# Performance work log

Measured on AMD Instinct MI355X. Metric: run time of the kernel, lower is better.

## Reference

```python
import jax, jax.numpy as jnp
import numpy as np

AABB0 = np.array([-1.5, -1.5, -1.5], np.float32)
AABB1 = np.array([1.5, 1.5, 1.5], np.float32)
GRID = (300, 300, 300)
NEAR, FAR = 2.0, 6.0
STEP = float(np.mean((AABB1 - AABB0) / (np.array(GRID, np.float32) - 1)) * 0.5)  # step_ratio=0.5
DIST_SCALE = 25.0
DENSITY_SHIFT = -10.0
W_THRES = 1e-4
PE = 2  # view_pe = feat_pe = 2
MAT = ((0, 1), (0, 2), (1, 2))
VEC = (2, 1, 0)
N_RAYS, N_SAMP = 1024, 512
DN, AN = 16, 16
APP_DIM, FEAT_C = 27, 128
IN_MLP = 2 * PE * 3 + 2 * PE * APP_DIM + 3 + APP_DIM  # 150


def posenc(x, freqs):
    fb = (2.0 ** jnp.arange(freqs)).astype(x.dtype)
    p = (x[..., None] * fb).reshape(x.shape[:-1] + (x.shape[-1] * freqs,))
    return jnp.concatenate([jnp.sin(p), jnp.cos(p)], -1)


def bilinear2d(plane, xy):
    # plane [C,H,W]; xy [P,2] in [-1,1], x->W, y->H; align_corners=True, border clamp
    C, H, W = plane.shape
    x = jnp.clip((xy[:, 0] * 0.5 + 0.5) * (W - 1), 0.0, W - 1)
    y = jnp.clip((xy[:, 1] * 0.5 + 0.5) * (H - 1), 0.0, H - 1)
    x0 = jnp.clip(jnp.floor(x), 0, W - 2).astype(jnp.int32)
    y0 = jnp.clip(jnp.floor(y), 0, H - 2).astype(jnp.int32)
    wx, wy = x - x0, y - y0
    v00 = plane[:, y0, x0]
    v01 = plane[:, y0, x0 + 1]
    v10 = plane[:, y0 + 1, x0]
    v11 = plane[:, y0 + 1, x0 + 1]
    return (v00 * (1 - wx) + v01 * wx) * (1 - wy) + (v10 * (1 - wx) + v11 * wx) * wy  # [C,P]


def linear1d(line, z):
    # line [C,L]; z [P] in [-1,1]
    C, L = line.shape
    t = jnp.clip((z * 0.5 + 0.5) * (L - 1), 0.0, L - 1)
    i0 = jnp.clip(jnp.floor(t), 0, L - 2).astype(jnp.int32)
    w = t - i0
    return line[:, i0] * (1 - w) + line[:, i0 + 1] * w  # [C,P]


def _forward(rays_o, rays_d, dplanes, dlines, aplanes, alines, basis_w,
             w1, b1, w2, b2, w3, b3, n_samples):
    a0, a1 = jnp.asarray(AABB0), jnp.asarray(AABB1)
    # --- sample_ray (is_train=False) ---
    vec = jnp.where(rays_d == 0, 1e-6, rays_d)
    rate_a = (a1 - rays_o) / vec
    rate_b = (a0 - rays_o) / vec
    t_min = jnp.clip(jnp.max(jnp.minimum(rate_a, rate_b), -1), NEAR, FAR)  # [R]
    rng = jnp.arange(n_samples, dtype=rays_o.dtype)[None]
    z_vals = t_min[:, None] + STEP * rng  # [R,S]
    pts = rays_o[:, None, :] + rays_d[:, None, :] * z_vals[..., None]  # [R,S,3]
    ray_valid = jnp.all((pts >= a0) & (pts <= a1), -1)  # [R,S]
    xn = ((pts - a0) * (2.0 / (a1 - a0)) - 1.0).reshape(-1, 3)  # normalize_coord -> [P,3]
    # --- density: VM decomposition (sum of plane*line products) ---
    sigma_feat = jnp.zeros((xn.shape[0],), xn.dtype)
    for i in range(3):
        p = bilinear2d(dplanes[i], xn[:, jnp.array(MAT[i])])
        l = linear1d(dlines[i], xn[:, VEC[i]])
        sigma_feat = sigma_feat + jnp.sum(p * l, 0)
    sigma = jax.nn.softplus(sigma_feat + DENSITY_SHIFT).reshape(z_vals.shape)
    sigma = jnp.where(ray_valid, sigma, 0.0)
    # --- raw2alpha compositing ---
    dists = jnp.concatenate([z_vals[:, 1:] - z_vals[:, :-1], jnp.zeros_like(z_vals[:, :1])], -1)
    alpha = 1.0 - jnp.exp(-sigma * dists * DIST_SCALE)
    T = jnp.cumprod(jnp.concatenate([jnp.ones_like(alpha[:, :1]), 1.0 - alpha + 1e-10], -1), -1)
    weight = alpha * T[:, :-1]
    app_mask = weight > W_THRES
    # --- appearance features + basis_mat ---
    coefs = [bilinear2d(aplanes[i], xn[:, jnp.array(MAT[i])]) * linear1d(alines[i], xn[:, VEC[i]])
             for i in range(3)]
    feat = jnp.concatenate(coefs, 0).T @ basis_w.T  # [P, app_dim]
    view = jnp.broadcast_to(rays_d[:, None, :], pts.shape).reshape(-1, 3)
    # --- MLPRender_Fea: [features, viewdirs, posenc(features), posenc(viewdirs)] ---
    mlp_in = jnp.concatenate([feat, view, posenc(feat, PE), posenc(view, PE)], -1)
    h = jax.nn.relu(mlp_in @ w1.T + b1)
    h = jax.nn.relu(h @ w2.T + b2)
    rgb = jax.nn.sigmoid(h @ w3.T + b3).reshape(z_vals.shape + (3,))
    rgb = jnp.where(app_mask[..., None], rgb, 0.0)
    acc = jnp.sum(weight, -1)
    rgb_map = jnp.sum(weight[..., None] * rgb, 1)
    rgb_map = jnp.clip(rgb_map + (1.0 - acc)[:, None], 0.0, 1.0)  # white background
    depth_map = jnp.sum(weight * z_vals, -1)
    return rgb_map, depth_map


def setup_inputs() -> dict:
    key = jax.random.key(0)
    ks = jax.random.split(key, 20)
    rd = jax.random.normal(ks[0], (N_RAYS, 3), jnp.float32)
    rays_d = rd / jnp.linalg.norm(rd, axis=-1, keepdims=True)
    rays_o = -3.0 * rays_d + 0.1 * jax.random.normal(ks[1], (N_RAYS, 3), jnp.float32)
    inp = {"rays_o": rays_o, "rays_d": rays_d}
    for i, ((m0, m1), v) in enumerate(zip(MAT, VEC)):
        inp[f"dplane{i}"] = jax.random.normal(ks[2 + i], (DN, GRID[m1], GRID[m0]), jnp.float32)
        inp[f"dline{i}"] = jax.random.normal(ks[5 + i], (DN, GRID[v]), jnp.float32)
        inp[f"aplane{i}"] = 0.1 * jax.random.normal(ks[8 + i], (AN, GRID[m1], GRID[m0]), jnp.float32)
        inp[f"aline{i}"] = 0.1 * jax.random.normal(ks[11 + i], (AN, GRID[v]), jnp.float32)
    inp["basis_w"] = 0.1 * jax.random.normal(ks[14], (APP_DIM, 3 * AN), jnp.float32)
    inp["w1"] = 0.05 * jax.random.normal(ks[15], (FEAT_C, IN_MLP), jnp.float32)
    inp["b1"] = jnp.zeros((FEAT_C,), jnp.float32)
    inp["w2"] = 0.05 * jax.random.normal(ks[16], (FEAT_C, FEAT_C), jnp.float32)
    inp["b2"] = jnp.zeros((FEAT_C,), jnp.float32)
    inp["w3"] = 0.05 * jax.random.normal(ks[17], (3, FEAT_C), jnp.float32)
    inp["b3"] = jnp.zeros((3,), jnp.float32)
    inp["n_samples"] = N_SAMP
    return inp


def reference(rays_o, rays_d, dplane0, dplane1, dplane2, dline0, dline1, dline2,
              aplane0, aplane1, aplane2, aline0, aline1, aline2, basis_w,
              w1, b1, w2, b2, w3, b3, n_samples):
    return _forward(rays_o, rays_d, (dplane0, dplane1, dplane2), (dline0, dline1, dline2),
                    (aplane0, aplane1, aplane2), (aline0, aline1, aline2), basis_w,
                    w1, b1, w2, b2, w3, b3, n_samples)
```

## Files before the change

kernel.cpp:

```cpp
#include <hip/hip_runtime.h>
#include <hip/hip_fp16.h>
#include <math.h>

#define NRAYS 1024
#define NSAMP 512
#define GRIDN 300
#define POS_ELEMS (GRIDN*GRIDN)
#define PLANE_ELEMS (16*POS_ELEMS)
#define CMAX 524288

typedef short bf16x8 __attribute__((ext_vector_type(8)));
typedef short short8 __attribute__((ext_vector_type(8)));
typedef float f32x4  __attribute__((ext_vector_type(4)));

struct H8v { __half2 h[4]; };

__device__ __forceinline__ float clampf(float x, float a, float b){ return fminf(fmaxf(x,a),b); }
__device__ __forceinline__ unsigned short f2b(float f){
    unsigned u = __builtin_bit_cast(unsigned, f);
    u = (u + 0x7FFFu + ((u>>16)&1u)) >> 16;
    return (unsigned short)u;
}
__device__ __forceinline__ float b2f(unsigned short h){
    unsigned u = ((unsigned)h) << 16;
    return __builtin_bit_cast(float, u);
}

__device__ __forceinline__ float ray_tmin(float o0,float o1,float o2,float d0,float d1,float d2){
    float v0=(d0==0.f)?1e-6f:d0, v1=(d1==0.f)?1e-6f:d1, v2=(d2==0.f)?1e-6f:d2;
    float t_min = -1e30f, a, b;
    a=(1.5f-o0)/v0; b=(-1.5f-o0)/v0; t_min=fmaxf(t_min,fminf(a,b));
    a=(1.5f-o1)/v1; b=(-1.5f-o1)/v1; t_min=fmaxf(t_min,fminf(a,b));
    a=(1.5f-o2)/v2; b=(-1.5f-o2)/v2; t_min=fmaxf(t_min,fminf(a,b));
    return clampf(t_min, 2.0f, 6.0f);
}

struct TPtrs {
    const float* psrc[6]; __half* pdst[6];
    const float* lsrc[6]; __half* ldst[6];
};

__global__ __launch_bounds__(256) void k_transpose(TPtrs tp) {
    int by  = blockIdx.y;
    int pos = blockIdx.x * 256 + threadIdx.x;
    if (pos < POS_ELEMS) {
        const float* src = tp.psrc[by];
        __half2 o[8];
        #pragma unroll
        for (int e = 0; e < 8; e++) {
            float a = src[(2*e  ) * POS_ELEMS + pos];
            float b = src[(2*e+1) * POS_ELEMS + pos];
            o[e] = __float22half2_rn(make_float2(a,b));
        }
        float4* dst = (float4*)(tp.pdst[by] + (size_t)pos * 16);
        dst[0] = *(float4*)&o[0];
        dst[1] = *(float4*)&o[4];
    }
    if (pos < GRIDN) {
        const float* ls = tp.lsrc[by];
        __half*      ld = tp.ldst[by];
        #pragma unroll
        for (int c = 0; c < 16; c++) ld[pos * 16 + c] = __float2half_rn(ls[c * GRIDN + pos]);
    }
}

__global__ __launch_bounds__(256) void k_prepw(
    const float* __restrict__ w1, const float* __restrict__ w2,
    unsigned short* __restrict__ w1b, unsigned short* __restrict__ w2b)
{
    int idx = blockIdx.x * 256 + threadIdx.x;
    if (idx < 128*160) {
        int j = idx / 160, k = idx - j*160;
        w1b[idx] = (k < 150) ? f2b(w1[j*150 + k]) : 0;
    } else if (idx < 128*160 + 128*128) {
        int i2 = idx - 128*160;
        w2b[i2] = f2b(w2[i2]);
    }
}

__global__ __launch_bounds__(256) void k_alpha(
    const float* __restrict__ ro, const float* __restrict__ rd,
    const __half* __restrict__ dpT0, const __half* __restrict__ dpT1, const __half* __restrict__ dpT2,
    const __half* __restrict__ dlT0, const __half* __restrict__ dlT1, const __half* __restrict__ dlT2,
    float* __restrict__ alpha_out)
{
    const float STEPF = (3.0f/299.0f)*0.5f;
    int id = blockIdx.x*256 + threadIdx.x;
    int r = id >> 9, s = id & (NSAMP-1);

    float o0=ro[r*3+0], o1=ro[r*3+1], o2=ro[r*3+2];
    float d0=rd[r*3+0], d1=rd[r*3+1], d2=rd[r*3+2];
    float t_min = ray_tmin(o0,o1,o2,d0,d1,d2);

    float z  = t_min + STEPF * (float)s;
    float p0 = o0 + d0*z, p1 = o1 + d1*z, p2 = o2 + d2*z;
    bool valid = (p0>=-1.5f)&&(p0<=1.5f)&&(p1>=-1.5f)&&(p1<=1.5f)&&(p2>=-1.5f)&&(p2<=1.5f);

    float sig = 0.f;
    if (valid) {
        float xn[3] = { (p0+1.5f)*(2.0f/3.0f)-1.0f,
                        (p1+1.5f)*(2.0f/3.0f)-1.0f,
                        (p2+1.5f)*(2.0f/3.0f)-1.0f };
        const __half* dpT[3] = {dpT0,dpT1,dpT2};
        const __half* dlT[3] = {dlT0,dlT1,dlT2};
        const int M0[3]={0,0,1}, M1[3]={1,2,2}, V[3]={2,1,0};
        float sf = 0.f;
        #pragma unroll
        for (int i=0;i<3;i++) {
            float fx = clampf((xn[M0[i]]*0.5f+0.5f)*299.f, 0.f, 299.f);
            float fy = clampf((xn[M1[i]]*0.5f+0.5f)*299.f, 0.f, 299.f);
            float ft = clampf((xn[V[i]] *0.5f+0.5f)*299.f, 0.f, 299.f);
            int x0=min((int)fx,298), y0=min((int)fy,298), i0=min((int)ft,298);
            float wx=fx-(float)x0, wy=fy-(float)y0, wt=ft-(float)i0;
            const H8v* r0 = (const H8v*)(dpT[i] + (size_t)( y0   *GRIDN+x0)*16);
            const H8v* r1 = (const H8v*)(dpT[i] + (size_t)((y0+1)*GRIDN+x0)*16);
            const H8v* lp = (const H8v*)(dlT[i] + (size_t)i0*16);
            H8v a0[4] = {r0[0],r0[1],r0[2],r0[3]};
            H8v a1[4] = {r1[0],r1[1],r1[2],r1[3]};
            H8v lv[4] = {lp[0],lp[1],lp[2],lp[3]};
            #pragma unroll
            for (int cb=0; cb<2; cb++) {
                #pragma unroll
                for (int e=0; e<4; e++) {
                    float2 c00 = __half22float2(a0[cb  ].h[e]);
                    float2 c01 = __half22float2(a0[cb+2].h[e]);
                    float2 c10 = __half22float2(a1[cb  ].h[e]);
                    float2 c11 = __half22float2(a1[cb+2].h[e]);
                    float2 l0  = __half22float2(lv[cb  ].h[e]);
                    float2 l1  = __half22float2(lv[cb+2].h[e]);
                    float bx = (c00.x*(1.f-wx)+c01.x*wx)*(1.f-wy) + (c10.x*(1.f-wx)+c11.x*wx)*wy;
                    float by = (c00.y*(1.f-wx)+c01.y*wx)*(1.f-wy) + (c10.y*(1.f-wx)+c11.y*wx)*wy;
                    float lx = l0.x*(1.f-wt)+l1.x*wt;
                    float ly = l0.y*(1.f-wt)+l1.y*wt;
                    sf += bx*lx + by*ly;
                }
            }
        }
        float xs = sf - 10.0f;
        sig = fmaxf(xs, 0.f) + __logf(1.f + __expf(-fabsf(xs)));
    }
    alpha_out[id] = (s < NSAMP-1) ? (1.f - __expf(-sig * (STEPF*25.0f))) : 0.f;
}

__global__ __launch_bounds__(256) void k_scan(
    const float* __restrict__ ro, const float* __restrict__ rd,
    const float* __restrict__ alpha_in,
    float* __restrict__ acc_out, float* __restrict__ depth_out,
    int* __restrict__ tmpl, float* __restrict__ tmpw, int* __restrict__ cnt)
{
    const float STEPF = (3.0f/299.0f)*0.5f;
    int r = blockIdx.x;
    int tid = threadIdx.x;
    int lane = tid & 63, wv = tid >> 6;

    float o0=ro[r*3+0], o1=ro[r*3+1], o2=ro[r*3+2];
    float d0=rd[r*3+0], d1=rd[r*3+1], d2=rd[r*3+2];
    float t_min = ray_tmin(o0,o1,o2,d0,d1,d2);

    float2 av = *(const float2*)&alpha_in[r*NSAMP + 2*tid];
    float aj0 = av.x, aj1 = av.y;
    float zj0 = t_min + STEPF * (float)(2*tid);
    float zj1 = t_min + STEPF * (float)(2*tid+1);

    float v0 = (1.f - aj0) + 1e-10f;
    float v1 = (1.f - aj1) + 1e-10f;
    float inc = v0 * v1;
    #pragma unroll
    for (int off=1; off<64; off<<=1) {
        float t = __shfl_up(inc, off, 64);
        if (lane >= off) inc *= t;
    }
    __shared__ float wtot[4], swsum[4], sdep[4];
    __shared__ int   wcnt[4];
    if (lane == 63) wtot[wv] = inc;
    __syncthreads();
    float pre = 1.f;
    for (int i=0;i<wv;i++) pre *= wtot[i];
    float excl = __shfl_up(inc, 1, 64);
    if (lane == 0) excl = 1.f;
    float T0 = pre * excl;
    float w0 = aj0 * T0;
    float w1 = aj1 * T0 * v0;

    float rw = w0 + w1, rz = w0*zj0 + w1*zj1;
    #pragma unroll
    for (int off=32; off>0; off>>=1) { rw += __shfl_xor(rw,off,64); rz += __shfl_xor(rz,off,64); }
    if (lane == 0) { swsum[wv] = rw; sdep[wv] = rz; }

    bool act0 = (w0 > 1e-4f), act1 = (w1 > 1e-4f);
    unsigned long long m0 = __ballot(act0);
    unsigned long long m1 = __ballot(act1);
    int tot = __popcll(m0) + __popcll(m1);
    if (lane == 0) wcnt[wv] = tot;
    __syncthreads();
    int base = 0;
    for (int i=0;i<wv;i++) base += wcnt[i];
    unsigned long long below = (1ull<<lane)-1ull;
    int o = base + __popcll(m0 & below) + __popcll(m1 & below);
    int* tl = tmpl + r*NSAMP;
    float* tw = tmpw + r*NSAMP;
    if (act0) { tl[o] = (r<<9)|(2*tid);   tw[o] = w0; o++; }
    if (act1) { tl[o] = (r<<9)|(2*tid+1); tw[o] = w1; }

    if (tid == 0) {
        float a=0.f, b=0.f;
        #pragma unroll
        for (int i=0;i<4;i++){ a+=swsum[i]; b+=sdep[i]; }
        acc_out[r] = a; depth_out[r] = b;
        cnt[r] = wcnt[0]+wcnt[1]+wcnt[2]+wcnt[3];
    }
}

__global__ __launch_bounds__(1024) void k_prefix(
    const int* __restrict__ cnt, int* __restrict__ basep, int* __restrict__ counter)
{
    int tid = threadIdx.x;
    int lane = tid & 63, wv = tid >> 6;
    int v = cnt[tid];
    int inc = v;
    #pragma unroll
    for (int off=1; off<64; off<<=1) {
        int t = __shfl_up(inc, off, 64);
        if (lane >= off) inc += t;
    }
    __shared__ int wsum[16];
    if (lane == 63) wsum[wv] = inc;
    __syncthreads();
    int pre = 0;
    for (int i=0;i<wv;i++) pre += wsum[i];
    basep[tid] = pre + inc - v;
    if (tid == 1023) *counter = pre + inc;
}

__global__ __launch_bounds__(256) void k_compact(
    const int* __restrict__ tmpl, const float* __restrict__ tmpw,
    const int* __restrict__ cnt, const int* __restrict__ basep,
    int* __restrict__ list, float* __restrict__ wlist)
{
    int r = blockIdx.x;
    int n = cnt[r], b = basep[r];
    const int* tl = tmpl + r*NSAMP;
    const float* tw = tmpw + r*NSAMP;
    for (int j = threadIdx.x; j < n; j += 256) {
        list[b+j]  = tl[j];
        wlist[b+j] = tw[j];
    }
}

__global__ __launch_bounds__(256) void k_gather(
    const float* __restrict__ ro, const float* __restrict__ rd,
    const __half* __restrict__ apT0, const __half* __restrict__ apT1, const __half* __restrict__ apT2,
    const __half* __restrict__ alT0, const __half* __restrict__ alT1, const __half* __restrict__ alT2,
    const float* __restrict__ basis_w,
    const int* __restrict__ list, const int* __restrict__ counter,
    float* __restrict__ Xf)
{
    const float STEPF = (3.0f/299.0f)*0.5f;
    int gid = blockIdx.x*256 + threadIdx.x;
    int idx = gid >> 3, q = gid & 7;
    int count = *counter;
    if (idx >= count) return;

    int sid = list[idx];
    int r = sid >> 9, s = sid & (NSAMP-1);
    float o0=ro[r*3+0], o1=ro[r*3+1], o2=ro[r*3+2];
    float d0=rd[r*3+0], d1=rd[r*3+1], d2=rd[r*3+2];
    float t_min = ray_tmin(o0,o1,o2,d0,d1,d2);
    float z = t_min + STEPF*(float)s;
    float xn[3] = { ((o0+d0*z)+1.5f)*(2.0f/3.0f)-1.0f,
                    ((o1+d1*z)+1.5f)*(2.0f/3.0f)-1.0f,
                    ((o2+d2*z)+1.5f)*(2.0f/3.0f)-1.0f };

    bool active = (q < 6);
    int i = min(q >> 1, 2);
    int h = q & 1;

    float c8[8];
    {
        const __half* apT[3]={apT0,apT1,apT2};
        const __half* alT[3]={alT0,alT1,alT2};
        const int M0[3]={0,0,1}, M1[3]={1,2,2}, V[3]={2,1,0};
        float fx = clampf((xn[M0[i]]*0.5f+0.5f)*299.f, 0.f, 299.f);
        float fy = clampf((xn[M1[i]]*0.5f+0.5f)*299.f, 0.f, 299.f);
        float ft = clampf((xn[V[i]] *0.5f+0.5f)*299.f, 0.f, 299.f);
        int x0=min((int)fx,298), y0=min((int)fy,298), i0=min((int)ft,298);
        float wx=fx-(float)x0, wy=fy-(float)y0, wt=ft-(float)i0;
        __half2 w00=__float2half2_rn((1.f-wx)*(1.f-wy)), w01=__float2half2_rn(wx*(1.f-wy));
        __half2 w10=__float2half2_rn((1.f-wx)*wy),       w11=__float2half2_rn(wx*wy);
        __half2 u0 =__float2half2_rn(1.f-wt),            u1 =__float2half2_rn(wt);
        if (active) {
            const __half* base = apT[i] + (size_t)(y0*GRIDN+x0)*16 + h*8;
            H8v a00 = *(const H8v*)(base);
            H8v a01 = *(const H8v*)(base + 16);
            H8v a10 = *(const H8v*)(base + GRIDN*16);
            H8v a11 = *(const H8v*)(base + GRIDN*16 + 16);
            const __half* lb = alT[i] + (size_t)i0*16 + h*8;
            H8v l0 = *(const H8v*)(lb);
            H8v l1 = *(const H8v*)(lb + 16);
            #pragma unroll
            for (int e=0;e<4;e++) {
                __half2 p = __hmul2(a00.h[e],w00);
                p = __hfma2(a01.h[e],w01,p);
                p = __hfma2(a10.h[e],w10,p);
                p = __hfma2(a11.h[e],w11,p);
                __half2 l = __hmul2(l0.h[e],u0);
                l = __hfma2(l1.h[e],u1,l);
                float2 c = __half22float2(__hmul2(p,l));
                c8[2*e]   = c.x;
                c8[2*e+1] = c.y;
            }
        } else {
            #pragma unroll
            for (int e=0;e<8;e++) c8[e] = 0.f;
        }
    }

    float kv[4] = {0.f, 0.f, 0.f, 0.f};
    #pragma unroll
    for (int j=0;j<27;j++) {
        const float4* b4 = (const float4*)(basis_w + j*48 + i*16 + h*8);
        float4 b0 = b4[0], b1 = b4[1];
        float p = b0.x*c8[0] + b0.y*c8[1] + b0.z*c8[2] + b0.w*c8[3]
                + b1.x*c8[4] + b1.y*c8[5] + b1.z*c8[6] + b1.w*c8[7];
        p += __shfl_xor(p, 1, 64);
        p += __shfl_xor(p, 2, 64);
        p += __shfl_xor(p, 4, 64);
        if (q == (j >> 2)) kv[j & 3] = p;
    }

    float4 v = make_float4(kv[0], kv[1], kv[2], kv[3]);
    if (q == 6) v.w = d0;
    if (q == 7) { v = make_float4(d1, d2, 0.f, 0.f); }
    *(float4*)&Xf[(size_t)idx*32 + q*4] = v;
}

#define XST 168
#define HST 136
#define TIL 32
#define XFS 36

__global__ __launch_bounds__(512, 4) void k_gemm(
    const float* __restrict__ Xf,
    const unsigned short* __restrict__ w1b, const float* __restrict__ b1p,
    const unsigned short* __restrict__ w2b, const float* __restrict__ b2p,
    const float* __restrict__ w3p, const float* __restrict__ b3p,
    const float* __restrict__ wlist, const int* __restrict__ counter,
    __half* __restrict__ contrib)
{
    __shared__ __align__(16) unsigned short Xs[TIL*XST];
    __shared__ __align__(16) unsigned short Hs[TIL*HST];
    __shared__ __align__(16) float Xf_s[TIL][XFS];

    int tid  = threadIdx.x;
    int wvid = tid >> 6, lane = tid & 63, ln15 = lane & 15, kq = lane >> 4;

    int count  = *counter;
    int ntiles = (count + TIL-1) >> 5;
    if ((int)blockIdx.x >= ntiles) return;

    int jrow = (wvid<<4) + ln15;
    bf16x8 w1f[5], w2f[4];
    #pragma unroll
    for (int ks=0; ks<5; ks++)
        w1f[ks] = *(const bf16x8*)&w1b[jrow*160 + ks*32 + kq*8];
    #pragma unroll
    for (int ks=0; ks<4; ks++)
        w2f[ks] = *(const bf16x8*)&w2b[jrow*128 + ks*32 + kq*8];
    float bias1 = b1p[jrow];
    float bias2 = b2p[jrow];

    for (int t = blockIdx.x; t < ntiles; t += gridDim.x) {
        if (tid < TIL*8) {
            int row = tid >> 3, q = tid & 7;
            int idx = t*TIL + row;
            float4 v = make_float4(0.f,0.f,0.f,0.f);
            if (idx < count) v = *(const float4*)&Xf[(size_t)idx*32 + q*4];
            *(float4*)&Xf_s[row][q*4] = v;
        }
        __syncthreads();

        for (int u = tid; u < TIL*30; u += 512) {
            int row = u / 30, j = u - row*30;
            unsigned short* X = &Xs[row*XST];
            float f = Xf_s[row][j];
            float s1 = __sinf(f), s2 = __sinf(2.f*f);
            float c1 = __cosf(f), c2 = __cosf(2.f*f);
            X[j] = f2b(f);
            int c = j - 27;
            int o_s = (j < 27) ? (30 + 2*j) : (138 + 2*c);
            int o_c = (j < 27) ? (84 + 2*j) : (144 + 2*c);
            X[o_s]   = f2b(s1); X[o_s+1] = f2b(s2);
            X[o_c]   = f2b(c1); X[o_c+1] = f2b(c2);
        }
        for (int u = tid; u < TIL*10; u += 512) {
            int row = u / 10, k = 150 + (u - row*10);
            Xs[row*XST + k] = 0;
        }
        __syncthreads();

        {
            f32x4 acc[2] = {};
            #pragma unroll
            for (int ks=0; ks<5; ks++) {
                int ko = ks*32 + kq*8;
                #pragma unroll
                for (int m=0;m<2;m++) {
                    bf16x8 a = *(const bf16x8*)&Xs[(m*16 + ln15)*XST + ko];
                    acc[m] = __builtin_amdgcn_mfma_f32_16x16x32_bf16(a, w1f[ks], acc[m], 0,0,0);
                }
            }
            int col = jrow;
            #pragma unroll
            for (int m=0;m<2;m++) {
                int rbase = m*16 + kq*4;
                #pragma unroll
                for (int j=0;j<4;j++)
                    Hs[(rbase+j)*HST + col] = f2b(fmaxf(acc[m][j] + bias1, 0.f));
            }
        }
        __syncthreads();

        {
            f32x4 acc[2] = {};
            #pragma unroll
            for (int ks=0; ks<4; ks++) {
                int ko = ks*32 + kq*8;
                #pragma unroll
                for (int m=0;m<2;m++) {
                    bf16x8 a = *(const bf16x8*)&Hs[(m*16 + ln15)*HST + ko];
                    acc[m] = __builtin_amdgcn_mfma_f32_16x16x32_bf16(a, w2f[ks], acc[m], 0,0,0);
                }
            }
            int col = jrow;
            #pragma unroll
            for (int m=0;m<2;m++) {
                int rbase = m*16 + kq*4;
                #pragma unroll
                for (int j=0;j<4;j++)
                    Xs[(rbase+j)*HST + col] = f2b(fmaxf(acc[m][j] + bias2, 0.f));
            }
        }
        __syncthreads();

        if (tid < TIL*8) {
            int u = tid >> 3, q = tid & 7;
            int idx = t*TIL + u;
            if (q < 6 && idx < count) {
                int ch = q >> 1, hf = q & 1;
                float wgt = wlist[idx];
                const unsigned short* h2 = Xs + u*HST + hf*64;
                const float* wr = w3p + ch*128 + hf*64;
                float p = 0.f;
                #pragma unroll
                for (int k=0;k<64;k+=8) {
                    bf16x8 hv = *(const bf16x8*)&h2[k];
                    #pragma unroll
                    for (int e=0;e<8;e++)
                        p += b2f((unsigned short)hv[e]) * wr[k+e];
                }
                p += __shfl_xor(p, 1, 64);
                if (hf == 0) {
                    float v = 0.f;
                    if (wgt > 0.f) {
                        float acc5 = b3p[ch] + p;
                        v = wgt * (1.f/(1.f + __expf(-acc5)));
                    }
                    contrib[(size_t)ch*CMAX + idx] = __float2half(v);
                }
            }
        }
        __syncthreads();
    }
}

__global__ __launch_bounds__(128) void k_rgbsum(
    const __half* __restrict__ contrib,
    const int* __restrict__ cnt, const int* __restrict__ basep,
    float* __restrict__ rgbacc)
{
    int r = blockIdx.x;
    int n = cnt[r], b = basep[r];
    int tid = threadIdx.x, lane = tid & 63, w = tid >> 6;
    float s0=0.f, s1=0.f, s2=0.f;
    for (int j = tid; j < n; j += 128) {
        s0 += __half2float(contrib[0*CMAX + b + j]);
        s1 += __half2float(contrib[1*CMAX + b + j]);
        s2 += __half2float(contrib[2*CMAX + b + j]);
    }
    #pragma unroll
    for (int off=32; off>0; off>>=1) {
        s0 += __shfl_xor(s0,off,64); s1 += __shfl_xor(s1,off,64); s2 += __shfl_xor(s2,off,64);
    }
    __shared__ float sh[3][2];
    if (lane == 0) { sh[0][w]=s0; sh[1][w]=s1; sh[2][w]=s2; }
    __syncthreads();
    if (tid == 0) {
        rgbacc[r*3+0] = sh[0][0]+sh[0][1];
        rgbacc[r*3+1] = sh[1][0]+sh[1][1];
        rgbacc[r*3+2] = sh[2][0]+sh[2][1];
    }
}

__global__ __launch_bounds__(256) void k_final(
    const float* __restrict__ rgbacc, const float* __restrict__ acc_out, float* __restrict__ out)
{
    int i = blockIdx.x*256 + threadIdx.x;
    if (i < NRAYS*3) {
        int r = i/3;
        out[i] = clampf(rgbacc[i] + (1.f - acc_out[r]), 0.f, 1.f);
    }
}

extern "C" void kernel_launch(void* const* d_in, const int* in_sizes, int n_in,
                              void* d_out, int out_size, void* d_ws, size_t ws_size,
                              hipStream_t stream)
{
    const float* ro = (const float*)d_in[0];
    const float* rd = (const float*)d_in[1];
    const float* dplane[3] = {(const float*)d_in[2],(const float*)d_in[6],(const float*)d_in[10]};
    const float* dline[3]  = {(const float*)d_in[3],(const float*)d_in[7],(const float*)d_in[11]};
    const float* aplane[3] = {(const float*)d_in[4],(const float*)d_in[8],(const float*)d_in[12]};
    const float* aline[3]  = {(const float*)d_in[5],(const float*)d_in[9],(const float*)d_in[13]};
    const float* basis_w = (const float*)d_in[14];
    const float* w1 = (const float*)d_in[15];
    const float* b1 = (const float*)d_in[16];
    const float* w2 = (const float*)d_in[17];
    const float* b2 = (const float*)d_in[18];
    const float* w3 = (const float*)d_in[19];
    const float* b3 = (const float*)d_in[20];
    float* out = (float*)d_out;

    char* ws = (char*)d_ws;
    int*    counter  = (int*)   (ws + 0);
    float*  rgbacc   = (float*) (ws + 256);
    float*  accb     = (float*) (ws + 12544);
    float*  wlist    = (float*) (ws + 16640);
    int*    list     = (int*)   (ws + 2113792);
    __half* planesT  = (__half*)(ws + 4210944);
    __half* linesT   = (__half*)(ws + 21490944);
    unsigned short* w1b = (unsigned short*)(ws + 21548544);
    unsigned short* w2b = (unsigned short*)(ws + 21589504);
    float*  alphab   = (float*) (ws + 21622272);
    int*    cntb     = (int*)   (ws + 23719424);
    int*    baseb    = (int*)   (ws + 23723520);
    int*    tmpl     = (int*)   (ws + 23727616);
    float*  tmpw     = (float*) (ws + 25824768);
    __half* contrib  = (__half*)(ws + 23727616);
    float*  Xf       = (float*) (ws + 27921920);


    TPtrs tp;
    for (int i=0;i<3;i++) {
        tp.psrc[i]   = dplane[i]; tp.pdst[i]   = planesT + (size_t)i*PLANE_ELEMS;
        tp.psrc[3+i] = aplane[i]; tp.pdst[3+i] = planesT + (size_t)(3+i)*PLANE_ELEMS;
        tp.lsrc[i]   = dline[i];  tp.ldst[i]   = linesT + i*(GRIDN*16);
        tp.lsrc[3+i] = aline[i];  tp.ldst[3+i] = linesT + (3+i)*(GRIDN*16);
    }
    dim3 tg((POS_ELEMS+255)/256, 6);
    hipLaunchKernelGGL(k_transpose, tg, dim3(256), 0, stream, tp);

    k_prepw<<<(128*160 + 128*128 + 255)/256, 256, 0, stream>>>(w1, w2, w1b, w2b);

    k_alpha<<<(NRAYS*NSAMP)/256, 256, 0, stream>>>(
        ro, rd,
        planesT + 0*(size_t)PLANE_ELEMS, planesT + 1*(size_t)PLANE_ELEMS, planesT + 2*(size_t)PLANE_ELEMS,
        linesT + 0*(GRIDN*16), linesT + 1*(GRIDN*16), linesT + 2*(GRIDN*16),
        alphab);

    k_scan<<<NRAYS, 256, 0, stream>>>(
        ro, rd, alphab, accb, out + NRAYS*3, tmpl, tmpw, cntb);

    k_prefix<<<1, 1024, 0, stream>>>(cntb, baseb, counter);

    k_compact<<<NRAYS, 256, 0, stream>>>(tmpl, tmpw, cntb, baseb, list, wlist);

    k_gather<<<(CMAX*8)/256, 256, 0, stream>>>(
        ro, rd,
        planesT + 3*(size_t)PLANE_ELEMS, planesT + 4*(size_t)PLANE_ELEMS, planesT + 5*(size_t)PLANE_ELEMS,
        linesT + 3*(GRIDN*16), linesT + 4*(GRIDN*16), linesT + 5*(GRIDN*16),
        basis_w, list, counter, Xf);

    k_gemm<<<4096, 512, 0, stream>>>(
        Xf, w1b, b1, w2b, b2, w3, b3,
        wlist, counter, contrib);

    k_rgbsum<<<NRAYS, 128, 0, stream>>>(contrib, cntb, baseb, rgbacc);

    k_final<<<(NRAYS*3+255)/256, 256, 0, stream>>>(rgbacc, accb, out);
}
```

Before: 114.2 us.

## Split density sampling across two threads per sample with packed half math

The density alpha kernel now uses two threads per sample, each handling 8 of the 16 channels, and combines their partial sums with a lane shuffle. Bilinear and linear interpolation now run in packed half2 FMAs with precomputed corner weights instead of fp32 after conversion. The goal is more memory-level parallelism and fewer instructions per sample on the gather-heavy kernel. The cost is doubled launch size, recomputed ray setup per thread, and lower precision from half-precision accumulation of the interpolated features.

```diff
diff --git a/kernel.cpp b/kernel.cpp
--- a/kernel.cpp
+++ b/kernel.cpp
@@ -85,7 +85,8 @@
     float* __restrict__ alpha_out)
 {
     const float STEPF = (3.0f/299.0f)*0.5f;
-    int id = blockIdx.x*256 + threadIdx.x;
+    int gid = blockIdx.x*256 + threadIdx.x;
+    int id = gid >> 1, h = gid & 1;
     int r = id >> 9, s = id & (NSAMP-1);
 
     float o0=ro[r*3+0], o1=ro[r*3+1], o2=ro[r*3+2];
@@ -96,7 +97,7 @@
     float p0 = o0 + d0*z, p1 = o1 + d1*z, p2 = o2 + d2*z;
     bool valid = (p0>=-1.5f)&&(p0<=1.5f)&&(p1>=-1.5f)&&(p1<=1.5f)&&(p2>=-1.5f)&&(p2<=1.5f);
 
-    float sig = 0.f;
+    float sfp = 0.f;
     if (valid) {
         float xn[3] = { (p0+1.5f)*(2.0f/3.0f)-1.0f,
                         (p1+1.5f)*(2.0f/3.0f)-1.0f,
@@ -104,7 +105,6 @@
         const __half* dpT[3] = {dpT0,dpT1,dpT2};
         const __half* dlT[3] = {dlT0,dlT1,dlT2};
         const int M0[3]={0,0,1}, M1[3]={1,2,2}, V[3]={2,1,0};
-        float sf = 0.f;
         #pragma unroll
         for (int i=0;i<3;i++) {
             float fx = clampf((xn[M0[i]]*0.5f+0.5f)*299.f, 0.f, 299.f);
@@ -112,34 +112,39 @@
             float ft = clampf((xn[V[i]] *0.5f+0.5f)*299.f, 0.f, 299.f);
             int x0=min((int)fx,298), y0=min((int)fy,298), i0=min((int)ft,298);
             float wx=fx-(float)x0, wy=fy-(float)y0, wt=ft-(float)i0;
-            const H8v* r0 = (const H8v*)(dpT[i] + (size_t)( y0   *GRIDN+x0)*16);
-            const H8v* r1 = (const H8v*)(dpT[i] + (size_t)((y0+1)*GRIDN+x0)*16);
-            const H8v* lp = (const H8v*)(dlT[i] + (size_t)i0*16);
-            H8v a0[4] = {r0[0],r0[1],r0[2],r0[3]};
-            H8v a1[4] = {r1[0],r1[1],r1[2],r1[3]};
-            H8v lv[4] = {lp[0],lp[1],lp[2],lp[3]};
-            #pragma unroll
-            for (int cb=0; cb<2; cb++) {
-                #pragma unroll
-                for (int e=0; e<4; e++) {
-                    float2 c00 = __half22float2(a0[cb  ].h[e]);
-                    float2 c01 = __half22float2(a0[cb+2].h[e]);
-                    float2 c10 = __half22float2(a1[cb  ].h[e]);
-                    float2 c11 = __half22float2(a1[cb+2].h[e]);
-                    float2 l0  = __half22float2(lv[cb  ].h[e]);
-                    float2 l1  = __half22float2(lv[cb+2].h[e]);
-                    float bx = (c00.x*(1.f-wx)+c01.x*wx)*(1.f-wy) + (c10.x*(1.f-wx)+c11.x*wx)*wy;
-                    float by = (c00.y*(1.f-wx)+c01.y*wx)*(1.f-wy) + (c10.y*(1.f-wx)+c11.y*wx)*wy;
-                    float lx = l0.x*(1.f-wt)+l1.x*wt;
-                    float ly = l0.y*(1.f-wt)+l1.y*wt;
-                    sf += bx*lx + by*ly;
-                }
-            }
-        }
-        float xs = sf - 10.0f;
-        sig = fmaxf(xs, 0.f) + __logf(1.f + __expf(-fabsf(xs)));
-    }
-    alpha_out[id] = (s < NSAMP-1) ? (1.f - __expf(-sig * (STEPF*25.0f))) : 0.f;
+            __half2 w00=__float2half2_rn((1.f-wx)*(1.f-wy)), w01=__float2half2_rn(wx*(1.f-wy));
+            __half2 w10=__float2half2_rn((1.f-wx)*wy),       w11=__float2half2_rn(wx*wy);
+            __half2 u0 =__float2half2_rn(1.f-wt),            u1 =__float2half2_rn(wt);
+            const __half* base = dpT[i] + (size_t)(y0*GRIDN+x0)*16 + h*8;
+            H8v a00 = *(const H8v*)(base);
+            H8v a01 = *(const H8v*)(base + 16);
+            H8v a10 = *(const H8v*)(base + GRIDN*16);
+            H8v a11 = *(const H8v*)(base + GRIDN*16 + 16);
+            const __half* lb = dlT[i] + (size_t)i0*16 + h*8;
+            H8v l0 = *(const H8v*)(lb);
+            H8v l1 = *(const H8v*)(lb + 16);
+            #pragma unroll
+            for (int e=0;e<4;e++) {
+                __half2 p = __hmul2(a00.h[e],w00);
+                p = __hfma2(a01.h[e],w01,p);
+                p = __hfma2(a10.h[e],w10,p);
+                p = __hfma2(a11.h[e],w11,p);
+                __half2 l = __hmul2(l0.h[e],u0);
+                l = __hfma2(l1.h[e],u1,l);
+                float2 c = __half22float2(__hmul2(p,l));
+                sfp += c.x + c.y;
+            }
+        }
+    }
+    float sf = sfp + __shfl_xor(sfp, 1, 64);
+    if (h == 0) {
+        float sig = 0.f;
+        if (valid) {
+            float xs = sf - 10.0f;
+            sig = fmaxf(xs, 0.f) + __logf(1.f + __expf(-fabsf(xs)));
+        }
+        alpha_out[id] = (s < NSAMP-1) ? (1.f - __expf(-sig * (STEPF*25.0f))) : 0.f;
+    }
 }
 
 __global__ __launch_bounds__(256) void k_scan(
@@ -561,7 +566,7 @@
 
     k_prepw<<<(128*160 + 128*128 + 255)/256, 256, 0, stream>>>(w1, w2, w1b, w2b);
 
-    k_alpha<<<(NRAYS*NSAMP)/256, 256, 0, stream>>>(
+    k_alpha<<<(NRAYS*NSAMP*2)/256, 256, 0, stream>>>(
         ro, rd,
         planesT + 0*(size_t)PLANE_ELEMS, planesT + 1*(size_t)PLANE_ELEMS, planesT + 2*(size_t)PLANE_ELEMS,
         linesT + 0*(GRIDN*16), linesT + 1*(GRIDN*16), linesT + 2*(GRIDN*16),
```

Measured after the change: 109.1 us. 4.4% less time.
